# Kernel optimization log

Hardware: AMD Instinct MI355X
Metric: run time of the kernel (lower is better)

The kernel has to match this reference:

```python
import jax, jax.numpy as jnp
import numpy as np

NUM_EXPERTS = 64
TOP_K = 2
NOISE_STD = 0.1


def setup_inputs() -> dict:
    key = jax.random.key(0)
    k1, k2, k3 = jax.random.split(key, 3)
    x = jax.random.normal(k1, (8192, 4096), dtype=jnp.float32)
    W = jax.random.normal(k2, (NUM_EXPERTS, 4096), dtype=jnp.float32) * 0.01  # nn.init.normal_(std=0.01)
    noise = jax.random.normal(k3, (8192, NUM_EXPERTS), dtype=jnp.float32)
    return {"x": x, "W": W, "noise": noise}


def reference(x, W, noise):
    batch = x.shape[0]
    # router_logits = x @ W^T  -> [batch, num_experts]
    router_logits = jnp.einsum("bd,ed->be", x, W)
    noisy_logits = router_logits + NOISE_STD * noise  # training=True path
    top_k_logits, top_k_indices = jax.lax.top_k(noisy_logits, TOP_K)
    expert_weights = jax.nn.softmax(top_k_logits, axis=-1)
    # load balancing loss (Switch Transformer): one_hot(sel).sum over k and batch
    # replaced by scatter-add counts per expert
    counts = jnp.zeros((NUM_EXPERTS,), dtype=jnp.float32).at[top_k_indices.reshape(-1)].add(1.0)
    fraction_tokens = counts / batch
    router_probs = jax.nn.softmax(router_logits, axis=-1)
    mean_router_prob = router_probs.mean(axis=0)
    load_balance_loss = NUM_EXPERTS * jnp.sum(fraction_tokens * mean_router_prob)
    return (top_k_indices, expert_weights, router_logits, load_balance_loss)
```

## Files before the change

kernel.cpp:

```cpp
#include <hip/hip_runtime.h>
#include <hip/hip_bf16.h>

#define BATCH 8192
#define DMODEL 4096
#define NEXP 64

typedef __attribute__((ext_vector_type(8))) short short8;
typedef __attribute__((ext_vector_type(4))) float f32x4;

#define WF_FLOATS  393216

#define GLD16(dst_lds, src_g)                                                  \
    __builtin_amdgcn_global_load_lds(                                          \
        (const __attribute__((address_space(1))) void*)(src_g),                \
        (__attribute__((address_space(3))) void*)(dst_lds), 16, 0, 0)

__global__ __launch_bounds__(256) void build_wf(const float* __restrict__ W,
                                                unsigned short* __restrict__ WF2)
{
    const int gid = blockIdx.x * 256 + threadIdx.x;
    const int ks = gid >> 8;
    const int cf = (gid >> 6) & 3;
    const int l  = gid & 63;
    const int e  = cf * 16 + (l & 15);
    const int k0 = ks * 32 + (l >> 4) * 8;
    const float* src = W + (size_t)e * DMODEL + k0;

    short8 hv, mv, lv;
#pragma unroll
    for (int j = 0; j < 8; ++j) {
        const float xv = src[j];
        const __hip_bfloat16 h = __float2bfloat16(xv);
        const float r1 = xv - __bfloat162float(h);
        const __hip_bfloat16 m = __float2bfloat16(r1);
        const float r2 = r1 - __bfloat162float(m);
        const __hip_bfloat16 lo = __float2bfloat16(r2);
        hv[j] = (short)__builtin_bit_cast(unsigned short, h);
        mv[j] = (short)__builtin_bit_cast(unsigned short, m);
        lv[j] = (short)__builtin_bit_cast(unsigned short, lo);
    }
    const size_t base = (size_t)ks * 6144 + cf * 512 + l * 8;
    *(short8*)&WF2[base]        = hv;
    *(short8*)&WF2[base + 2048] = mv;
    *(short8*)&WF2[base + 4096] = lv;
}


#define CVT1(V, J, AH, AM, AL) {                                              \
    const float xv_ = (V);                                                    \
    const __hip_bfloat16 h_ = __float2bfloat16(xv_);                          \
    const float r1_ = xv_ - __bfloat162float(h_);                             \
    const __hip_bfloat16 m_ = __float2bfloat16(r1_);                          \
    const float r2_ = r1_ - __bfloat162float(m_);                             \
    const __hip_bfloat16 l_ = __float2bfloat16(r2_);                          \
    AH[J] = (short)__builtin_bit_cast(unsigned short, h_);                    \
    AM[J] = (short)__builtin_bit_cast(unsigned short, m_);                    \
    AL[J] = (short)__builtin_bit_cast(unsigned short, l_); }

#define CVT8(X0, X1, AH, AM, AL)                                              \
    CVT1(X0[0], 0, AH, AM, AL) CVT1(X0[1], 1, AH, AM, AL)                     \
    CVT1(X0[2], 2, AH, AM, AL) CVT1(X0[3], 3, AH, AM, AL)                     \
    CVT1(X1[0], 4, AH, AM, AL) CVT1(X1[1], 5, AH, AM, AL)                     \
    CVT1(X1[2], 6, AH, AM, AL) CVT1(X1[3], 7, AH, AM, AL)

#define MFMA(A, B, C) __builtin_amdgcn_mfma_f32_16x16x32_bf16(A, B, C, 0, 0, 0)

__global__ __launch_bounds__(256, 4) void gemm_mfma(const float* __restrict__ x,
                                                    const unsigned short* __restrict__ WF2,
                                                    float* __restrict__ part,
                                                    int S)
{
    __shared__ float xs[2][2048];
    __shared__ unsigned short wsh[2][6144];

    const int t = threadIdx.x;
    const int l = t & 63;
    const int wid = t >> 6;
    const int g = blockIdx.x & 127;
    const int s = blockIdx.x >> 7;
    const int rowbase = g * 64;
    const int kbeg = s * (DMODEL / S);
    const int nsteps = (DMODEL / S) >> 5;

    const float* pxa[2];
#pragma unroll
    for (int r = 0; r < 2; ++r) {
        const int tr = wid * 16 + r * 8 + (l >> 3);
        const int ul = (l & 7) ^ (tr & 7);
        pxa[r] = x + (size_t)(rowbase + tr) * DMODEL + kbeg + ul * 4;
    }
    const unsigned short* pwb = WF2 + (size_t)(kbeg >> 5) * 6144 + t * 8;

#define STAGE(BUF, IT) {                                                       \
    _Pragma("unroll")                                                          \
    for (int r_ = 0; r_ < 2; ++r_)                                             \
        GLD16(&xs[BUF][wid * 512 + r_ * 256], pxa[r_] + (size_t)(IT) * 32);    \
    _Pragma("unroll")                                                          \
    for (int r_ = 0; r_ < 3; ++r_)                                             \
        GLD16(&wsh[BUF][r_ * 2048 + wid * 512],                                \
              pwb + (size_t)(IT) * 6144 + r_ * 2048); }

    const int lr = l & 15;
    const int lk = l >> 4;
    const int xr = lr & 7;
    const int trw = wid * 16 + lr;
    const int a0 = trw * 32 + (((lk * 2)     ^ xr) * 4);
    const int a1 = trw * 32 + (((lk * 2 + 1) ^ xr) * 4);

    f32x4 acc[4] = {};

    STAGE(0, 0)

    for (int it = 0; it < nsteps; ++it) {
        const int cur = it & 1;
        if (it + 1 < nsteps) {
            STAGE(cur ^ 1, it + 1)
            asm volatile("s_waitcnt vmcnt(5)" ::: "memory");
        } else {
            asm volatile("s_waitcnt vmcnt(0)" ::: "memory");
        }
        __builtin_amdgcn_s_barrier();

        const f32x4 xa0 = *(const f32x4*)&xs[cur][a0];
        const f32x4 xa1 = *(const f32x4*)&xs[cur][a1];
        short8 ah, am, al;
        CVT8(xa0, xa1, ah, am, al)

#pragma unroll
        for (int cf = 0; cf < 4; ++cf) {
            const unsigned short* wp = &wsh[cur][cf * 512 + l * 8];
            const short8 bh = *(const short8*)(wp);
            const short8 bm = *(const short8*)(wp + 2048);
            const short8 bl = *(const short8*)(wp + 4096);
            acc[cf] = MFMA(ah, bh, acc[cf]);
            acc[cf] = MFMA(ah, bm, acc[cf]);
            acc[cf] = MFMA(am, bh, acc[cf]);
            acc[cf] = MFMA(ah, bl, acc[cf]);
            acc[cf] = MFMA(al, bh, acc[cf]);
            acc[cf] = MFMA(am, bm, acc[cf]);
        }
        __builtin_amdgcn_s_barrier();
    }

    const int orow = lk * 4;
#pragma unroll
    for (int j = 0; j < 4; ++j) {
        const int row = rowbase + wid * 16 + orow + j;
        float* dst = part + ((size_t)s * BATCH + row) * NEXP + lr;
#pragma unroll
        for (int cf = 0; cf < 4; ++cf)
            dst[cf * 16] = acc[cf][j];
    }
#undef STAGE
}

template<int NS>
__global__ __launch_bounds__(256) void router2(const float* __restrict__ part,
                                               const float* __restrict__ noise,
                                               float* __restrict__ out,
                                               float* __restrict__ probsum,
                                               float* __restrict__ counts,
                                               int* __restrict__ done)
{
    __shared__ float sps[4][64];
    __shared__ float scnt[4][64];
    __shared__ int lastFlag;

    const int t = threadIdx.x;
    const int w = t >> 6;
    const int lane = t & 63;
    const int wg = blockIdx.x * 4 + w;

    float* out_idx = out;
    float* out_w = out + 16384;
    float* out_logits = out + 32768;

    float psum_local = 0.f;
    float cnt_local = 0.f;

    for (int r = 0; r < 8; ++r) {
        const int row = wg * 8 + r;
        float lgt = 0.f;
#pragma unroll
        for (int s = 0; s < NS; ++s)
            lgt += part[((size_t)s * BATCH + row) * NEXP + lane];
        out_logits[(size_t)row * NEXP + lane] = lgt;

        const float ny = lgt + 0.1f * noise[(size_t)row * NEXP + lane];

        float v1 = ny; int i1 = lane;
#pragma unroll
        for (int m = 32; m >= 1; m >>= 1) {
            float ov = __shfl_xor(v1, m);
            int oi = __shfl_xor(i1, m);
            if (ov > v1 || (ov == v1 && oi < i1)) { v1 = ov; i1 = oi; }
        }
        float v2 = (lane == i1) ? -1e30f : ny; int i2 = lane;
#pragma unroll
        for (int m = 32; m >= 1; m >>= 1) {
            float ov = __shfl_xor(v2, m);
            int oi = __shfl_xor(i2, m);
            if (ov > v2 || (ov == v2 && oi < i2)) { v2 = ov; i2 = oi; }
        }

        if (lane == 0) {
            const float d = expf(v2 - v1);
            const float w1 = 1.0f / (1.0f + d);
            out_idx[row * 2 + 0] = (float)i1;
            out_idx[row * 2 + 1] = (float)i2;
            out_w[row * 2 + 0] = w1;
            out_w[row * 2 + 1] = 1.0f - w1;
        }

        float m = lgt;
#pragma unroll
        for (int ss = 32; ss >= 1; ss >>= 1) m = fmaxf(m, __shfl_xor(m, ss));
        const float p = expf(lgt - m);
        float sum = p;
#pragma unroll
        for (int ss = 32; ss >= 1; ss >>= 1) sum += __shfl_xor(sum, ss);
        psum_local += p / sum;
        cnt_local += (lane == i1 ? 1.f : 0.f) + (lane == i2 ? 1.f : 0.f);
    }

    sps[w][lane] = psum_local;
    scnt[w][lane] = cnt_local;
    __syncthreads();
    if (t < 64) {
        float ssum = 0.f, c = 0.f;
#pragma unroll
        for (int ww = 0; ww < 4; ++ww) { ssum += sps[ww][t]; c += scnt[ww][t]; }
        atomicAdd(&probsum[t], ssum);
        atomicAdd(&counts[t], c);
    }
    __syncthreads();
    if (t == 0) {
        __threadfence();
        lastFlag = (atomicAdd(done, 1) == (int)gridDim.x - 1) ? 1 : 0;
    }
    __syncthreads();
    if (lastFlag && t < 64) {
        const float ps = __hip_atomic_load(&probsum[t], __ATOMIC_RELAXED,
                                           __HIP_MEMORY_SCOPE_AGENT);
        const float ct = __hip_atomic_load(&counts[t], __ATOMIC_RELAXED,
                                           __HIP_MEMORY_SCOPE_AGENT);
        float v = ps * ct;
#pragma unroll
        for (int ss = 32; ss >= 1; ss >>= 1) v += __shfl_xor(v, ss);
        if (t == 0)
            out[557056] = (float)NEXP * v / ((float)BATCH * (float)BATCH);
    }
}

extern "C" void kernel_launch(void* const* d_in, const int* in_sizes, int n_in,
                              void* d_out, int out_size, void* d_ws, size_t ws_size,
                              hipStream_t stream)
{
    const float* x = (const float*)d_in[0];
    const float* W = (const float*)d_in[1];
    const float* noise = (const float*)d_in[2];
    float* out = (float*)d_out;
    float* ws = (float*)d_ws;

    float* probsum = ws;
    float* counts = ws + 64;
    int* done = (int*)(ws + 128);
    unsigned short* WF2 = (unsigned short*)(ws + 256);
    float* part = ws + 256 + WF_FLOATS;

    int S = 1;
    const size_t base_floats = 256 + WF_FLOATS;
    for (int cand = 8; cand >= 1; cand >>= 1) {
        const size_t need = (base_floats + (size_t)cand * BATCH * NEXP) * sizeof(float);
        if (ws_size >= need) { S = cand; break; }
    }

    hipMemsetAsync(d_ws, 0, 1024, stream);

    build_wf<<<128, 256, 0, stream>>>(W, WF2);
    gemm_mfma<<<128 * S, 256, 0, stream>>>(x, WF2, part, S);
    switch (S) {
        case 8: router2<8><<<256, 256, 0, stream>>>(part, noise, out, probsum, counts, done); break;
        case 4: router2<4><<<256, 256, 0, stream>>>(part, noise, out, probsum, counts, done); break;
        case 2: router2<2><<<256, 256, 0, stream>>>(part, noise, out, probsum, counts, done); break;
        default: router2<1><<<256, 256, 0, stream>>>(part, noise, out, probsum, counts, done); break;
    }
}
```

Baseline: 65.45 us.

## Triple-buffer GEMM staging, cap split-K at 4, replace router atomics with per-block partials

The GEMM kernel moves from double to triple buffering of the x and W tiles in LDS, prefetching two steps ahead. Launch bounds are relaxed to 2 blocks per SM so the larger LDS footprint fits. Split-K is capped at 4, which halves the partial-sum traffic when the workspace would have allowed 8. In the router, the per-expert atomicAdds are replaced by per-block partial stores that the last block reduces deterministically, at the cost of extra workspace and a serial tail reduction.

```diff
diff --git a/kernel.cpp b/kernel.cpp
--- a/kernel.cpp
+++ b/kernel.cpp
@@ -65,13 +65,13 @@
 
 #define MFMA(A, B, C) __builtin_amdgcn_mfma_f32_16x16x32_bf16(A, B, C, 0, 0, 0)
 
-__global__ __launch_bounds__(256, 4) void gemm_mfma(const float* __restrict__ x,
+__global__ __launch_bounds__(256, 2) void gemm_mfma(const float* __restrict__ x,
                                                     const unsigned short* __restrict__ WF2,
                                                     float* __restrict__ part,
                                                     int S)
 {
-    __shared__ float xs[2][2048];
-    __shared__ unsigned short wsh[2][6144];
+    __shared__ float xs[3][2048];
+    __shared__ unsigned short wsh[3][6144];
 
     const int t = threadIdx.x;
     const int l = t & 63;
@@ -110,11 +110,15 @@
     f32x4 acc[4] = {};
 
     STAGE(0, 0)
-
+    STAGE(1, 1)
+
+    int cur = 0;
     for (int it = 0; it < nsteps; ++it) {
-        const int cur = it & 1;
-        if (it + 1 < nsteps) {
-            STAGE(cur ^ 1, it + 1)
+        if (it + 2 < nsteps) {
+            int nb = cur + 2; if (nb >= 3) nb -= 3;
+            STAGE(nb, it + 2)
+            asm volatile("s_waitcnt vmcnt(10)" ::: "memory");
+        } else if (it + 1 < nsteps) {
             asm volatile("s_waitcnt vmcnt(5)" ::: "memory");
         } else {
             asm volatile("s_waitcnt vmcnt(0)" ::: "memory");
@@ -140,6 +144,7 @@
             acc[cf] = MFMA(am, bm, acc[cf]);
         }
         __builtin_amdgcn_s_barrier();
+        cur = (cur + 1 == 3) ? 0 : cur + 1;
     }
 
     const int orow = lk * 4;
@@ -158,8 +163,8 @@
 __global__ __launch_bounds__(256) void router2(const float* __restrict__ part,
                                                const float* __restrict__ noise,
                                                float* __restrict__ out,
-                                               float* __restrict__ probsum,
-                                               float* __restrict__ counts,
+                                               float* __restrict__ bsum,
+                                               float* __restrict__ bcnt,
                                                int* __restrict__ done)
 {
     __shared__ float sps[4][64];
@@ -230,8 +235,10 @@
         float ssum = 0.f, c = 0.f;
 #pragma unroll
         for (int ww = 0; ww < 4; ++ww) { ssum += sps[ww][t]; c += scnt[ww][t]; }
-        atomicAdd(&probsum[t], ssum);
-        atomicAdd(&counts[t], c);
+        __hip_atomic_store(&bsum[(size_t)blockIdx.x * 64 + t], ssum,
+                           __ATOMIC_RELAXED, __HIP_MEMORY_SCOPE_AGENT);
+        __hip_atomic_store(&bcnt[(size_t)blockIdx.x * 64 + t], c,
+                           __ATOMIC_RELAXED, __HIP_MEMORY_SCOPE_AGENT);
     }
     __syncthreads();
     if (t == 0) {
@@ -239,12 +246,26 @@
         lastFlag = (atomicAdd(done, 1) == (int)gridDim.x - 1) ? 1 : 0;
     }
     __syncthreads();
-    if (lastFlag && t < 64) {
-        const float ps = __hip_atomic_load(&probsum[t], __ATOMIC_RELAXED,
-                                           __HIP_MEMORY_SCOPE_AGENT);
-        const float ct = __hip_atomic_load(&counts[t], __ATOMIC_RELAXED,
-                                           __HIP_MEMORY_SCOPE_AGENT);
-        float v = ps * ct;
+    if (!lastFlag) return;
+
+    __threadfence();
+    const int e = t & 63;
+    const int q = t >> 6;
+    float ps = 0.f, cs = 0.f;
+    for (int b = q; b < 256; b += 4) {
+        ps += __hip_atomic_load(&bsum[(size_t)b * 64 + e], __ATOMIC_RELAXED,
+                                __HIP_MEMORY_SCOPE_AGENT);
+        cs += __hip_atomic_load(&bcnt[(size_t)b * 64 + e], __ATOMIC_RELAXED,
+                                __HIP_MEMORY_SCOPE_AGENT);
+    }
+    sps[q][e] = ps;
+    scnt[q][e] = cs;
+    __syncthreads();
+    if (t < 64) {
+        float P = 0.f, C = 0.f;
+#pragma unroll
+        for (int ww = 0; ww < 4; ++ww) { P += sps[ww][t]; C += scnt[ww][t]; }
+        float v = P * C;
 #pragma unroll
         for (int ss = 32; ss >= 1; ss >>= 1) v += __shfl_xor(v, ss);
         if (t == 0)
@@ -262,27 +283,26 @@
     float* out = (float*)d_out;
     float* ws = (float*)d_ws;
 
-    float* probsum = ws;
-    float* counts = ws + 64;
-    int* done = (int*)(ws + 128);
+    int* done = (int*)ws;
     unsigned short* WF2 = (unsigned short*)(ws + 256);
-    float* part = ws + 256 + WF_FLOATS;
+    float* bsum = ws + 256 + WF_FLOATS;
+    float* bcnt = bsum + 16384;
+    float* part = bcnt + 16384;
 
     int S = 1;
-    const size_t base_floats = 256 + WF_FLOATS;
-    for (int cand = 8; cand >= 1; cand >>= 1) {
+    const size_t base_floats = 256 + WF_FLOATS + 32768;
+    for (int cand = 4; cand >= 1; cand >>= 1) {
         const size_t need = (base_floats + (size_t)cand * BATCH * NEXP) * sizeof(float);
         if (ws_size >= need) { S = cand; break; }
     }
 
-    hipMemsetAsync(d_ws, 0, 1024, stream);
+    hipMemsetAsync(d_ws, 0, 256, stream);
 
     build_wf<<<128, 256, 0, stream>>>(W, WF2);
     gemm_mfma<<<128 * S, 256, 0, stream>>>(x, WF2, part, S);
     switch (S) {
-        case 8: router2<8><<<256, 256, 0, stream>>>(part, noise, out, probsum, counts, done); break;
-        case 4: router2<4><<<256, 256, 0, stream>>>(part, noise, out, probsum, counts, done); break;
-        case 2: router2<2><<<256, 256, 0, stream>>>(part, noise, out, probsum, counts, done); break;
-        default: router2<1><<<256, 256, 0, stream>>>(part, noise, out, probsum, counts, done); break;
+        case 4: router2<4><<<256, 256, 0, stream>>>(part, noise, out, bsum, bcnt, done); break;
+        case 2: router2<2><<<256, 256, 0, stream>>>(part, noise, out, bsum, bcnt, done); break;
+        default: router2<1><<<256, 256, 0, stream>>>(part, noise, out, bsum, bcnt, done); break;
     }
 }
```

Measured after the change: 84.48 us. 1.29x slower.

## Fuse router epilogue into split-K GEMM via last-arriving-block counter

Applied to the files above, without the earlier changes.

The separate router kernel is merged into the GEMM. For each 64-row group, the last of the NS split-K blocks to finish (tracked with a per-group atomic counter) sums the partials and runs the top-2, softmax and load-balance reduction. The workspace memset is dropped by zeroing the counters inside build_wf block 0. This removes one kernel launch and the memset, but it adds fences and atomics, and the router work now runs inside the GEMM's occupancy-limited blocks.

```diff
diff --git a/kernel.cpp b/kernel.cpp
--- a/kernel.cpp
+++ b/kernel.cpp
@@ -16,9 +16,16 @@
         (__attribute__((address_space(3))) void*)(dst_lds), 16, 0, 0)
 
 __global__ __launch_bounds__(256) void build_wf(const float* __restrict__ W,
-                                                unsigned short* __restrict__ WF2)
+                                                unsigned short* __restrict__ WF2,
+                                                float* __restrict__ zbase)
 {
-    const int gid = blockIdx.x * 256 + threadIdx.x;
+    const int t = threadIdx.x;
+    if (blockIdx.x == 0) {
+        zbase[t] = 0.f;
+        zbase[t + 256] = 0.f;
+    }
+
+    const int gid = blockIdx.x * 256 + t;
     const int ks = gid >> 8;
     const int cf = (gid >> 6) & 3;
     const int l  = gid & 63;
@@ -65,13 +72,20 @@
 
 #define MFMA(A, B, C) __builtin_amdgcn_mfma_f32_16x16x32_bf16(A, B, C, 0, 0, 0)
 
-__global__ __launch_bounds__(256, 4) void gemm_mfma(const float* __restrict__ x,
-                                                    const unsigned short* __restrict__ WF2,
-                                                    float* __restrict__ part,
-                                                    int S)
+template<int NS>
+__global__ __launch_bounds__(256, 4) void gemm_fused(const float* __restrict__ x,
+                                                     const unsigned short* __restrict__ WF2,
+                                                     float* __restrict__ part,
+                                                     const float* __restrict__ noise,
+                                                     float* __restrict__ out,
+                                                     float* __restrict__ probsum,
+                                                     float* __restrict__ counts,
+                                                     int* __restrict__ gcnt,
+                                                     int* __restrict__ done)
 {
     __shared__ float xs[2][2048];
     __shared__ unsigned short wsh[2][6144];
+    __shared__ int routeFlag, lastFlag;
 
     const int t = threadIdx.x;
     const int l = t & 63;
@@ -79,8 +93,8 @@
     const int g = blockIdx.x & 127;
     const int s = blockIdx.x >> 7;
     const int rowbase = g * 64;
-    const int kbeg = s * (DMODEL / S);
-    const int nsteps = (DMODEL / S) >> 5;
+    const int kbeg = s * (DMODEL / NS);
+    const int nsteps = (DMODEL / NS) >> 5;
 
     const float* pxa[2];
 #pragma unroll
@@ -152,24 +166,17 @@
             dst[cf * 16] = acc[cf][j];
     }
 #undef STAGE
-}
-
-template<int NS>
-__global__ __launch_bounds__(256) void router2(const float* __restrict__ part,
-                                               const float* __restrict__ noise,
-                                               float* __restrict__ out,
-                                               float* __restrict__ probsum,
-                                               float* __restrict__ counts,
-                                               int* __restrict__ done)
-{
-    __shared__ float sps[4][64];
-    __shared__ float scnt[4][64];
-    __shared__ int lastFlag;
-
-    const int t = threadIdx.x;
-    const int w = t >> 6;
-    const int lane = t & 63;
-    const int wg = blockIdx.x * 4 + w;
+
+    __threadfence();
+    __syncthreads();
+    if (t == 0)
+        routeFlag = (atomicAdd(&gcnt[g], 1) == NS - 1) ? 1 : 0;
+    __syncthreads();
+    if (!routeFlag) return;
+    __threadfence();
+
+    float* sps  = &xs[0][0];
+    float* scnt = &xs[0][256];
 
     float* out_idx = out;
     float* out_w = out + 16384;
@@ -178,24 +185,24 @@
     float psum_local = 0.f;
     float cnt_local = 0.f;
 
-    for (int r = 0; r < 8; ++r) {
-        const int row = wg * 8 + r;
+    for (int r = 0; r < 16; ++r) {
+        const int row = rowbase + wid * 16 + r;
         float lgt = 0.f;
 #pragma unroll
-        for (int s = 0; s < NS; ++s)
-            lgt += part[((size_t)s * BATCH + row) * NEXP + lane];
-        out_logits[(size_t)row * NEXP + lane] = lgt;
-
-        const float ny = lgt + 0.1f * noise[(size_t)row * NEXP + lane];
-
-        float v1 = ny; int i1 = lane;
+        for (int ss = 0; ss < NS; ++ss)
+            lgt += part[((size_t)ss * BATCH + row) * NEXP + l];
+        out_logits[(size_t)row * NEXP + l] = lgt;
+
+        const float ny = lgt + 0.1f * noise[(size_t)row * NEXP + l];
+
+        float v1 = ny; int i1 = l;
 #pragma unroll
         for (int m = 32; m >= 1; m >>= 1) {
             float ov = __shfl_xor(v1, m);
             int oi = __shfl_xor(i1, m);
             if (ov > v1 || (ov == v1 && oi < i1)) { v1 = ov; i1 = oi; }
         }
-        float v2 = (lane == i1) ? -1e30f : ny; int i2 = lane;
+        float v2 = (l == i1) ? -1e30f : ny; int i2 = l;
 #pragma unroll
         for (int m = 32; m >= 1; m >>= 1) {
             float ov = __shfl_xor(v2, m);
@@ -203,7 +210,7 @@
             if (ov > v2 || (ov == v2 && oi < i2)) { v2 = ov; i2 = oi; }
         }
 
-        if (lane == 0) {
+        if (l == 0) {
             const float d = expf(v2 - v1);
             const float w1 = 1.0f / (1.0f + d);
             out_idx[row * 2 + 0] = (float)i1;
@@ -220,23 +227,23 @@
 #pragma unroll
         for (int ss = 32; ss >= 1; ss >>= 1) sum += __shfl_xor(sum, ss);
         psum_local += p / sum;
-        cnt_local += (lane == i1 ? 1.f : 0.f) + (lane == i2 ? 1.f : 0.f);
-    }
-
-    sps[w][lane] = psum_local;
-    scnt[w][lane] = cnt_local;
+        cnt_local += (l == i1 ? 1.f : 0.f) + (l == i2 ? 1.f : 0.f);
+    }
+
+    sps[wid * 64 + l] = psum_local;
+    scnt[wid * 64 + l] = cnt_local;
     __syncthreads();
     if (t < 64) {
         float ssum = 0.f, c = 0.f;
 #pragma unroll
-        for (int ww = 0; ww < 4; ++ww) { ssum += sps[ww][t]; c += scnt[ww][t]; }
+        for (int ww = 0; ww < 4; ++ww) { ssum += sps[ww * 64 + t]; c += scnt[ww * 64 + t]; }
         atomicAdd(&probsum[t], ssum);
         atomicAdd(&counts[t], c);
     }
     __syncthreads();
     if (t == 0) {
         __threadfence();
-        lastFlag = (atomicAdd(done, 1) == (int)gridDim.x - 1) ? 1 : 0;
+        lastFlag = (atomicAdd(done, 1) == 127) ? 1 : 0;
     }
     __syncthreads();
     if (lastFlag && t < 64) {
@@ -265,24 +272,23 @@
     float* probsum = ws;
     float* counts = ws + 64;
     int* done = (int*)(ws + 128);
-    unsigned short* WF2 = (unsigned short*)(ws + 256);
-    float* part = ws + 256 + WF_FLOATS;
+    int* gcnt = (int*)(ws + 192);
+    unsigned short* WF2 = (unsigned short*)(ws + 512);
+    float* part = ws + 512 + WF_FLOATS;
 
     int S = 1;
-    const size_t base_floats = 256 + WF_FLOATS;
+    const size_t base_floats = 512 + WF_FLOATS;
     for (int cand = 8; cand >= 1; cand >>= 1) {
         const size_t need = (base_floats + (size_t)cand * BATCH * NEXP) * sizeof(float);
         if (ws_size >= need) { S = cand; break; }
     }
 
-    hipMemsetAsync(d_ws, 0, 1024, stream);
-
-    build_wf<<<128, 256, 0, stream>>>(W, WF2);
-    gemm_mfma<<<128 * S, 256, 0, stream>>>(x, WF2, part, S);
+    build_wf<<<128, 256, 0, stream>>>(W, WF2, ws);
+
     switch (S) {
-        case 8: router2<8><<<256, 256, 0, stream>>>(part, noise, out, probsum, counts, done); break;
-        case 4: router2<4><<<256, 256, 0, stream>>>(part, noise, out, probsum, counts, done); break;
-        case 2: router2<2><<<256, 256, 0, stream>>>(part, noise, out, probsum, counts, done); break;
-        default: router2<1><<<256, 256, 0, stream>>>(part, noise, out, probsum, counts, done); break;
+        case 8: gemm_fused<8><<<128 * 8, 256, 0, stream>>>(x, WF2, part, noise, out, probsum, counts, gcnt, done); break;
+        case 4: gemm_fused<4><<<128 * 4, 256, 0, stream>>>(x, WF2, part, noise, out, probsum, counts, gcnt, done); break;
+        case 2: gemm_fused<2><<<128 * 2, 256, 0, stream>>>(x, WF2, part, noise, out, probsum, counts, gcnt, done); break;
+        default: gemm_fused<1><<<128 * 1, 256, 0, stream>>>(x, WF2, part, noise, out, probsum, counts, gcnt, done); break;
     }
 }
```

Result: slower. 203.4 us (+210.8%).
